# Optimization experiments

Measured on AMD Instinct MI355X. Metric: run time of the kernel, lower is better.

Reference implementation:

```python
import jax, jax.numpy as jnp
import numpy as np

NEG_SLOPE = 0.2  # PyG GATConv default negative_slope
EPS = 1e-16


def gat_conv(x, edge_index, W, att_src, att_dst, bias, heads, out_c, concat):
    """Faithful PyG GATConv forward (add_self_loops=True).
    x: [N, F_in], edge_index: [2, E] (row 0 = src, row 1 = dst),
    W: [heads*out_c, F_in], att_src/att_dst: [1, heads, out_c], bias: [out]
    """
    N = x.shape[0]
    loop = jnp.arange(N, dtype=edge_index.dtype)
    src = jnp.concatenate([edge_index[0], loop])
    dst = jnp.concatenate([edge_index[1], loop])

    h = (x @ W.T).reshape(N, heads, out_c)            # [N, H, C]
    a_src = jnp.sum(h * att_src, axis=-1)             # [N, H]
    a_dst = jnp.sum(h * att_dst, axis=-1)             # [N, H]

    e = jax.nn.leaky_relu(a_src[src] + a_dst[dst], NEG_SLOPE)   # [E+N, H]
    # numerically-stable segment softmax over incoming edges of dst
    m = jax.ops.segment_max(e, dst, num_segments=N)             # [N, H]
    p = jnp.exp(e - m[dst])
    denom = jax.ops.segment_sum(p, dst, num_segments=N)         # [N, H]
    alpha = p / (denom[dst] + EPS)                              # [E+N, H]

    out = jax.ops.segment_sum(h[src] * alpha[:, :, None], dst, num_segments=N)  # [N, H, C]
    out = out.reshape(N, heads * out_c) if concat else out.mean(axis=1)
    return out + bias


def setup_inputs() -> dict:
    key = jax.random.key(0)
    ks = jax.random.split(key, 11)
    N, E = 100_000, 1_600_000
    in_dim, hid, heads = 128, 64, 2
    s = 0.1
    x = jax.random.normal(ks[0], (N, in_dim), jnp.float32)
    edge_index_l2 = jax.random.randint(ks[1], (2, E), 0, N, dtype=jnp.int32)
    edge_index_l1 = jax.random.randint(ks[2], (2, E), 0, N, dtype=jnp.int32)
    # layer gat_l2: in_dim -> hid per head, heads=2, concat=True
    W2 = jax.random.normal(ks[3], (heads * hid, in_dim), jnp.float32) * s
    att_src2 = jax.random.normal(ks[4], (1, heads, hid), jnp.float32) * s
    att_dst2 = jax.random.normal(ks[5], (1, heads, hid), jnp.float32) * s
    b2 = jnp.zeros((heads * hid,), jnp.float32)
    # layer gat_l1: hid*heads -> hid, 1 head, concat=False
    W1 = jax.random.normal(ks[6], (hid, heads * hid), jnp.float32) * s
    att_src1 = jax.random.normal(ks[7], (1, 1, hid), jnp.float32) * s
    att_dst1 = jax.random.normal(ks[8], (1, 1, hid), jnp.float32) * s
    b1 = jnp.zeros((hid,), jnp.float32)
    return {
        "x": x,
        "edge_index_l1": edge_index_l1,
        "edge_index_l2": edge_index_l2,
        "W2": W2, "att_src2": att_src2, "att_dst2": att_dst2, "b2": b2,
        "W1": W1, "att_src1": att_src1, "att_dst1": att_dst1, "b1": b1,
    }


def reference(x, edge_index_l1, edge_index_l2, W2, att_src2, att_dst2, b2,
              W1, att_src1, att_dst1, b1):
    h = jax.nn.elu(gat_conv(x, edge_index_l2, W2, att_src2, att_dst2, b2,
                            heads=2, out_c=64, concat=True))    # [N, 128]
    h = jax.nn.elu(gat_conv(h, edge_index_l1, W1, att_src1, att_dst1, b1,
                            heads=1, out_c=64, concat=False))   # [N, 64]
    return h
```

## Files before the change

kernel.cpp:

```cpp
#include <hip/hip_runtime.h>
#include <hip/hip_bf16.h>
#include <math.h>

#define LRELU_SLOPE 0.2f
#define EPS 1e-16f
#define BUCK_SHIFT 8
#define BUCK_NODES 256
#define MAXBUCK 512

typedef __hip_bfloat16 bf16;
typedef __attribute__((ext_vector_type(8))) short bf16x8;
typedef __attribute__((ext_vector_type(4))) float f32x4;

__device__ inline float lrelu(float v) { return v > 0.f ? v : LRELU_SLOPE * v; }
__device__ inline float bflo(unsigned u) { return __uint_as_float(u << 16); }
__device__ inline float bfhi(unsigned u) { return __uint_as_float(u & 0xffff0000u); }
__device__ inline short f2bf(float f) {
  bf16 t = __float2bfloat16(f);
  return *reinterpret_cast<short*>(&t);
}

__global__ void convert_w(const float* __restrict__ W2, unsigned short* __restrict__ Wb2,
                          const float* __restrict__ W1, unsigned short* __restrict__ Wb1) {
  int idx = blockIdx.x * blockDim.x + threadIdx.x;
  if (idx < 16384) {
    Wb2[idx] = (unsigned short)f2bf(W2[idx]);
  } else {
    int i = idx - 16384;
    if (i < 8192) Wb1[i] = (unsigned short)f2bf(W1[i]);
  }
}

template <int EPB>
__global__ __launch_bounds__(256) void partition_kernel(const int* __restrict__ ei, int E,
                                                        int* __restrict__ gcur,
                                                        int2* __restrict__ part, int cap,
                                                        int nbuck) {
  __shared__ int cnt[MAXBUCK];
  __shared__ int sbase[MAXBUCK];
  const int tid = threadIdx.x;
  for (int t = tid; t < nbuck; t += 256) cnt[t] = 0;
  __syncthreads();
  const int e0 = blockIdx.x * EPB;
  constexpr int KPT = EPB / 256;
  int sv[KPT], dv[KPT];
#pragma unroll
  for (int k = 0; k < KPT; k++) {
    int e = e0 + tid + k * 256;
    if (e < E) {
      sv[k] = ei[e];
      dv[k] = ei[E + e];
      atomicAdd(&cnt[dv[k] >> BUCK_SHIFT], 1);
    } else {
      dv[k] = -1;
    }
  }
  __syncthreads();
  for (int t = tid; t < nbuck; t += 256) {
    int c = cnt[t];
    if (c) sbase[t] = atomicAdd(&gcur[t], c);
    cnt[t] = 0;
  }
  __syncthreads();
#pragma unroll
  for (int k = 0; k < KPT; k++) {
    if (dv[k] >= 0) {
      int b = dv[k] >> BUCK_SHIFT;
      int pos = sbase[b] + atomicAdd(&cnt[b], 1);
      if (pos < cap) part[(size_t)b * cap + pos] = make_int2(sv[k], dv[k]);
    }
  }
}

template <int H>
__global__ __launch_bounds__(256) void csr_build_kernel(
    const int2* __restrict__ part, const int* __restrict__ gcur, int cap,
    const float* __restrict__ asrc, const float* __restrict__ adst, int* __restrict__ eidx,
    float* __restrict__ pcsr, int* __restrict__ rowbeg, int* __restrict__ rowend, int N) {
  extern __shared__ char smem[];
  int* s_s = (int*)smem;
  unsigned short* s_d8 = (unsigned short*)(s_s + cap);
  int* hist = (int*)(s_d8 + cap);
  int* escan = hist + 256;
  int* cur = escan + 256;
  float* s_ad = (float*)(cur + 256);

  const int b = blockIdx.x;
  const int tid = threadIdx.x;
  const int nb0 = b << BUCK_SHIFT;
  const int nn = min(BUCK_NODES, N - nb0);
  const int cnt = min(gcur[b], cap);
  const int B = b * cap;

  hist[tid] = 0;
  cur[tid] = 0;
  for (int t = tid; t < nn * H; t += 256) s_ad[t] = adst[(size_t)nb0 * H + t];
  __syncthreads();
  for (int i = tid; i < cnt; i += 256) {
    int2 pr = part[(size_t)B + i];
    s_s[i] = pr.x;
    int d8 = pr.y & (BUCK_NODES - 1);
    s_d8[i] = (unsigned short)d8;
    atomicAdd(&hist[d8], 1);
  }
  __syncthreads();
  escan[tid] = hist[tid];
  __syncthreads();
  for (int off = 1; off < 256; off <<= 1) {
    int t = (tid >= off) ? escan[tid - off] : 0;
    __syncthreads();
    escan[tid] += t;
    __syncthreads();
  }
  if (tid < nn) {
    rowbeg[nb0 + tid] = B + escan[tid] - hist[tid];
    rowend[nb0 + tid] = B + escan[tid];
  }
  __syncthreads();
  for (int i = tid; i < cnt; i += 256) {
    int d8 = s_d8[i];
    int slot = B + (escan[d8] - hist[d8]) + atomicAdd(&cur[d8], 1);
    int s = s_s[i];
    eidx[slot] = s;
    if constexpr (H == 2) {
      float2 a = *(const float2*)&asrc[2 * (size_t)s];
      float2 ad = *(const float2*)&s_ad[2 * d8];
      float2 pv;
      pv.x = __expf(lrelu(a.x + ad.x));
      pv.y = __expf(lrelu(a.y + ad.y));
      *(float2*)&pcsr[2 * (size_t)slot] = pv;
    } else {
      pcsr[slot] = __expf(lrelu(asrc[s] + s_ad[d8]));
    }
  }
}

template <int M, int H, bool SPLIT, typename Tin>
__global__ __launch_bounds__(256) void gemm_att_mfma(
    const Tin* __restrict__ x, const unsigned short* __restrict__ Wb,
    const float* __restrict__ atts, const float* __restrict__ attd, bf16* __restrict__ h,
    float* __restrict__ asrc, float* __restrict__ adst, int N) {
  constexpr int K = 128;
  constexpr int NF = M / 16;
  const int wid = threadIdx.x >> 6;
  const int lane = threadIdx.x & 63;
  const int r0 = blockIdx.x * 64 + wid * 16;
  if (r0 >= N) return;
  const int colb = lane & 15;
  const int kgrp = lane >> 4;
  const size_t arow = (size_t)min(r0 + colb, N - 1);

  f32x4 acc[NF];
#pragma unroll
  for (int f = 0; f < NF; f++) acc[f] = (f32x4){0.f, 0.f, 0.f, 0.f};

#pragma unroll
  for (int k0 = 0; k0 < K; k0 += 32) {
    const int kb = k0 + kgrp * 8;
    bf16x8 ahi, alo;
    if constexpr (SPLIT) {
      const float* xp = (const float*)x + arow * K + kb;
      float4 l0 = *(const float4*)xp;
      float4 l1 = *(const float4*)(xp + 4);
      float xv[8] = {l0.x, l0.y, l0.z, l0.w, l1.x, l1.y, l1.z, l1.w};
#pragma unroll
      for (int j = 0; j < 8; j++) {
        short hb = f2bf(xv[j]);
        ahi[j] = hb;
        float hf = __uint_as_float(((unsigned)(unsigned short)hb) << 16);
        alo[j] = f2bf(xv[j] - hf);
      }
    } else {
      ahi = *(const bf16x8*)((const unsigned short*)x + arow * K + kb);
    }
#pragma unroll
    for (int f = 0; f < NF; f++) {
      bf16x8 b = *(const bf16x8*)(Wb + (size_t)(f * 16 + colb) * K + kb);
      if constexpr (SPLIT)
        acc[f] = __builtin_amdgcn_mfma_f32_16x16x32_bf16(alo, b, acc[f], 0, 0, 0);
      acc[f] = __builtin_amdgcn_mfma_f32_16x16x32_bf16(ahi, b, acc[f], 0, 0, 0);
    }
  }

#pragma unroll
  for (int r = 0; r < 4; r++) {
    const int row = r0 + kgrp * 4 + r;
    const bool ok = row < N;
    float s0 = 0.f, d0 = 0.f, s1 = 0.f, d1 = 0.f;
#pragma unroll
    for (int f = 0; f < NF; f++) {
      float v = acc[f][r];
      int c = f * 16 + colb;
      if (ok) h[(size_t)row * M + c] = __float2bfloat16(v);
      float av = atts[c], dv = attd[c];
      if (H == 2 && f >= NF / 2) {
        s1 += v * av;
        d1 += v * dv;
      } else {
        s0 += v * av;
        d0 += v * dv;
      }
    }
#pragma unroll
    for (int off = 1; off < 16; off <<= 1) {
      s0 += __shfl_xor(s0, off);
      d0 += __shfl_xor(d0, off);
      if (H == 2) {
        s1 += __shfl_xor(s1, off);
        d1 += __shfl_xor(d1, off);
      }
    }
    if (ok && colb == 0) {
      if (H == 2) {
        asrc[2 * (size_t)row] = s0;
        asrc[2 * (size_t)row + 1] = s1;
        adst[2 * (size_t)row] = d0;
        adst[2 * (size_t)row + 1] = d1;
      } else {
        asrc[row] = s0;
        adst[row] = d0;
      }
    }
  }
}

__global__ void gather2_kernel(const bf16* __restrict__ h, const float* __restrict__ asrc,
                               const float* __restrict__ adst, const int* __restrict__ rowbeg,
                               const int* __restrict__ rowend, const int* __restrict__ eidx,
                               const float2* __restrict__ pcsr, const float* __restrict__ bias,
                               bf16* __restrict__ outp, int N) {
  long long gt = (long long)blockIdx.x * blockDim.x + threadIdx.x;
  int n = (int)(gt >> 6);
  int lane = threadIdx.x & 63;
  if (n >= N) return;
  int start = rowbeg[n];
  int end = rowend[n];
  const float2 as = *(const float2*)&asrc[2 * (size_t)n];
  const float2 ad = *(const float2*)&adst[2 * (size_t)n];
  float p0 = __expf(lrelu(as.x + ad.x));
  float p1 = __expf(lrelu(as.y + ad.y));
  float den0 = p0, den1 = p1;
  const bool h0 = lane < 32;
  float p = h0 ? p0 : p1;
  unsigned hv = *(const unsigned*)&h[(size_t)n * 128 + 2 * lane];
  float acc0 = p * bflo(hv), acc1 = p * bfhi(hv);
  int j = start;
  for (; j + 3 < end; j += 4) {
    int sA = eidx[j], sB = eidx[j + 1], sC = eidx[j + 2], sD = eidx[j + 3];
    float2 pA = pcsr[j], pB = pcsr[j + 1], pC = pcsr[j + 2], pD = pcsr[j + 3];
    unsigned hA = *(const unsigned*)&h[(size_t)sA * 128 + 2 * lane];
    unsigned hB = *(const unsigned*)&h[(size_t)sB * 128 + 2 * lane];
    unsigned hC = *(const unsigned*)&h[(size_t)sC * 128 + 2 * lane];
    unsigned hD = *(const unsigned*)&h[(size_t)sD * 128 + 2 * lane];
    den0 += (pA.x + pB.x) + (pC.x + pD.x);
    den1 += (pA.y + pB.y) + (pC.y + pD.y);
    float pa = h0 ? pA.x : pA.y;
    float pb = h0 ? pB.x : pB.y;
    float pc = h0 ? pC.x : pC.y;
    float pd = h0 ? pD.x : pD.y;
    acc0 += (pa * bflo(hA) + pb * bflo(hB)) + (pc * bflo(hC) + pd * bflo(hD));
    acc1 += (pa * bfhi(hA) + pb * bfhi(hB)) + (pc * bfhi(hC) + pd * bfhi(hD));
  }
  for (; j < end; j++) {
    int sA = eidx[j];
    float2 pA = pcsr[j];
    unsigned hA = *(const unsigned*)&h[(size_t)sA * 128 + 2 * lane];
    den0 += pA.x;
    den1 += pA.y;
    float pa = h0 ? pA.x : pA.y;
    acc0 += pa * bflo(hA);
    acc1 += pa * bfhi(hA);
  }
  float den = (h0 ? den0 : den1) + EPS;
  int c = 2 * lane;
  float v0 = acc0 / den + bias[c];
  float v1 = acc1 / den + bias[c + 1];
  v0 = v0 > 0.f ? v0 : expm1f(v0);
  v1 = v1 > 0.f ? v1 : expm1f(v1);
  __hip_bfloat162 o;
  o.x = __float2bfloat16(v0);
  o.y = __float2bfloat16(v1);
  *(__hip_bfloat162*)&outp[(size_t)n * 128 + c] = o;
}

__global__ void gather1_kernel(const bf16* __restrict__ h, const float* __restrict__ asrc,
                               const float* __restrict__ adst, const int* __restrict__ rowbeg,
                               const int* __restrict__ rowend, const int* __restrict__ eidx,
                               const float* __restrict__ pcsr, const float* __restrict__ bias,
                               float* __restrict__ outp, int N) {
  long long gt = (long long)blockIdx.x * blockDim.x + threadIdx.x;
  int n = (int)(gt >> 6);
  int lane = threadIdx.x & 63;
  if (n >= N) return;
  int start = rowbeg[n];
  int end = rowend[n];
  float p = __expf(lrelu(asrc[n] + adst[n]));
  float den = p;
  float acc = p * __bfloat162float(h[(size_t)n * 64 + lane]);
  int j = start;
  for (; j + 3 < end; j += 4) {
    int sA = eidx[j], sB = eidx[j + 1], sC = eidx[j + 2], sD = eidx[j + 3];
    float pA = pcsr[j], pB = pcsr[j + 1], pC = pcsr[j + 2], pD = pcsr[j + 3];
    float hA = __bfloat162float(h[(size_t)sA * 64 + lane]);
    float hB = __bfloat162float(h[(size_t)sB * 64 + lane]);
    float hC = __bfloat162float(h[(size_t)sC * 64 + lane]);
    float hD = __bfloat162float(h[(size_t)sD * 64 + lane]);
    den += (pA + pB) + (pC + pD);
    acc += (pA * hA + pB * hB) + (pC * hC + pD * hD);
  }
  for (; j < end; j++) {
    int sA = eidx[j];
    float pA = pcsr[j];
    den += pA;
    acc += pA * __bfloat162float(h[(size_t)sA * 64 + lane]);
  }
  float v = acc / (den + EPS) + bias[lane];
  outp[(size_t)n * 64 + lane] = v > 0.f ? v : expm1f(v);
}

extern "C" void kernel_launch(void* const* d_in, const int* in_sizes, int n_in,
                              void* d_out, int out_size, void* d_ws, size_t ws_size,
                              hipStream_t stream) {
  const float* x = (const float*)d_in[0];
  const int* ei1 = (const int*)d_in[1];
  const int* ei2 = (const int*)d_in[2];
  const float* W2 = (const float*)d_in[3];
  const float* as2 = (const float*)d_in[4];
  const float* ad2 = (const float*)d_in[5];
  const float* b2 = (const float*)d_in[6];
  const float* W1 = (const float*)d_in[7];
  const float* as1 = (const float*)d_in[8];
  const float* ad1 = (const float*)d_in[9];
  const float* b1 = (const float*)d_in[10];
  float* out = (float*)d_out;

  const int N = in_sizes[0] / 128;
  const int E1 = in_sizes[1] / 2;
  const int E2 = in_sizes[2] / 2;
  const int Emax = E1 > E2 ? E1 : E2;
  const size_t Ns = (size_t)N;

  const int nbuck = (N + BUCK_NODES - 1) / BUCK_NODES;
  int lam = (Emax + nbuck - 1) / nbuck;
  int cap = lam + (lam >> 2) + 512;
  cap = (cap + 255) & ~(int)255;
  const size_t NC = (size_t)nbuck * cap;

  float* ws = (float*)d_ws;
  size_t o = 0;
  unsigned short* Wb2 = (unsigned short*)(ws + o); o += 8192;
  unsigned short* Wb1 = (unsigned short*)(ws + o); o += 4096;
  float* asrc2 = ws + o;  o += 2 * Ns;
  float* adst2 = ws + o;  o += 2 * Ns;
  float* asrc1 = ws + o;  o += Ns;
  float* adst1 = ws + o;  o += Ns;
  int* gcur2 = (int*)(ws + o);   o += (size_t)nbuck;
  int* gcur1 = (int*)(ws + o);   o += (size_t)nbuck;
  int* rowbeg2 = (int*)(ws + o); o += Ns;
  int* rowend2 = (int*)(ws + o); o += Ns;
  int* rowbeg1 = (int*)(ws + o); o += Ns;
  int* rowend1 = (int*)(ws + o); o += Ns;
  o = (o + 7) & ~(size_t)7;
  int2* part = (int2*)(ws + o);  o += 2 * NC;
  int* eidx = (int*)(ws + o);    o += NC;
  o = (o + 7) & ~(size_t)7;
  float* pcsr = ws + o;          o += 2 * NC;
  o = (o + 7) & ~(size_t)7;
  bf16* h2 = (bf16*)(ws + o);    o += 64 * Ns;
  bf16* h1 = h2;
  bf16* hin1 = (bf16*)(ws + o);  o += 64 * Ns;

  const size_t smem2 = (size_t)cap * 6 + 3 * 256 * 4 + 2 * 256 * 4 + 64;
  const size_t smem1 = (size_t)cap * 6 + 3 * 256 * 4 + 1 * 256 * 4 + 64;

  convert_w<<<(16384 + 8192 + 255) / 256, 256, 0, stream>>>(W2, Wb2, W1, Wb1);
  hipMemsetAsync(gcur2, 0, 2 * (size_t)nbuck * sizeof(int), stream);

  partition_kernel<4096><<<(E2 + 4095) / 4096, 256, 0, stream>>>(ei2, E2, gcur2, part, cap, nbuck);
  gemm_att_mfma<128, 2, true, float>
      <<<(N + 63) / 64, 256, 0, stream>>>(x, Wb2, as2, ad2, h2, asrc2, adst2, N);
  csr_build_kernel<2><<<nbuck, 256, smem2, stream>>>(part, gcur2, cap, asrc2, adst2, eidx, pcsr,
                                                     rowbeg2, rowend2, N);
  partition_kernel<4096><<<(E1 + 4095) / 4096, 256, 0, stream>>>(ei1, E1, gcur1, part, cap, nbuck);
  gather2_kernel<<<(N + 3) / 4, 256, 0, stream>>>(h2, asrc2, adst2, rowbeg2, rowend2, eidx,
                                                  (const float2*)pcsr, b2, hin1, N);

  gemm_att_mfma<64, 1, false, bf16>
      <<<(N + 63) / 64, 256, 0, stream>>>(hin1, Wb1, as1, ad1, h1, asrc1, adst1, N);
  csr_build_kernel<1><<<nbuck, 256, smem1, stream>>>(part, gcur1, cap, asrc1, adst1, eidx, pcsr,
                                                     rowbeg1, rowend1, N);
  gather1_kernel<<<(N + 3) / 4, 256, 0, stream>>>(h1, asrc1, adst1, rowbeg1, rowend1, eidx, pcsr,
                                                  b1, out, N);
}
```

Before: 343.1 us.

## Pack partition entries, pad CSR rows to eight, vectorize gathers

Partition entries are packed into a single int (src<<8 | local dst) instead of an int2, halving partition traffic and shared memory. CSR rows are padded to multiples of 8 with zero-weight dummy edges, so both gather kernels can use int4/float4 loads with no tail loop. The layer-1 gather now splits each wavefront into two halves over edges, with each lane handling two channels. Padding adds extra gather work and raises cap. Packing assumes source indices fit in 23 bits, and with cap reduced by 7*256 some edges may be dropped when a bucket overflows.

```diff
diff --git a/kernel.cpp b/kernel.cpp
--- a/kernel.cpp
+++ b/kernel.cpp
@@ -34,7 +34,7 @@
 template <int EPB>
 __global__ __launch_bounds__(256) void partition_kernel(const int* __restrict__ ei, int E,
                                                         int* __restrict__ gcur,
-                                                        int2* __restrict__ part, int cap,
+                                                        int* __restrict__ part, int cap,
                                                         int nbuck) {
   __shared__ int cnt[MAXBUCK];
   __shared__ int sbase[MAXBUCK];
@@ -67,29 +67,29 @@
     if (dv[k] >= 0) {
       int b = dv[k] >> BUCK_SHIFT;
       int pos = sbase[b] + atomicAdd(&cnt[b], 1);
-      if (pos < cap) part[(size_t)b * cap + pos] = make_int2(sv[k], dv[k]);
+      if (pos < cap) part[(size_t)b * cap + pos] = (sv[k] << 8) | (dv[k] & (BUCK_NODES - 1));
     }
   }
 }
 
 template <int H>
 __global__ __launch_bounds__(256) void csr_build_kernel(
-    const int2* __restrict__ part, const int* __restrict__ gcur, int cap,
+    const int* __restrict__ part, const int* __restrict__ gcur, int cap,
     const float* __restrict__ asrc, const float* __restrict__ adst, int* __restrict__ eidx,
     float* __restrict__ pcsr, int* __restrict__ rowbeg, int* __restrict__ rowend, int N) {
   extern __shared__ char smem[];
-  int* s_s = (int*)smem;
-  unsigned short* s_d8 = (unsigned short*)(s_s + cap);
-  int* hist = (int*)(s_d8 + cap);
-  int* escan = hist + 256;
-  int* cur = escan + 256;
+  int* s_sd = (int*)smem;
+  int* hist = (int*)(s_sd + cap);
+  int* histp = hist + 256;
+  int* escanp = histp + 256;
+  int* cur = escanp + 256;
   float* s_ad = (float*)(cur + 256);
 
   const int b = blockIdx.x;
   const int tid = threadIdx.x;
   const int nb0 = b << BUCK_SHIFT;
   const int nn = min(BUCK_NODES, N - nb0);
-  const int cnt = min(gcur[b], cap);
+  const int cnt = min(gcur[b], cap - 7 * BUCK_NODES);
   const int B = b * cap;
 
   hist[tid] = 0;
@@ -97,30 +97,31 @@
   for (int t = tid; t < nn * H; t += 256) s_ad[t] = adst[(size_t)nb0 * H + t];
   __syncthreads();
   for (int i = tid; i < cnt; i += 256) {
-    int2 pr = part[(size_t)B + i];
-    s_s[i] = pr.x;
-    int d8 = pr.y & (BUCK_NODES - 1);
-    s_d8[i] = (unsigned short)d8;
-    atomicAdd(&hist[d8], 1);
-  }
-  __syncthreads();
-  escan[tid] = hist[tid];
+    int pr = part[(size_t)B + i];
+    s_sd[i] = pr;
+    atomicAdd(&hist[pr & (BUCK_NODES - 1)], 1);
+  }
+  __syncthreads();
+  int hp = (hist[tid] + 7) & ~7;
+  histp[tid] = hp;
+  escanp[tid] = hp;
   __syncthreads();
   for (int off = 1; off < 256; off <<= 1) {
-    int t = (tid >= off) ? escan[tid - off] : 0;
+    int t = (tid >= off) ? escanp[tid - off] : 0;
     __syncthreads();
-    escan[tid] += t;
+    escanp[tid] += t;
     __syncthreads();
   }
   if (tid < nn) {
-    rowbeg[nb0 + tid] = B + escan[tid] - hist[tid];
-    rowend[nb0 + tid] = B + escan[tid];
+    rowbeg[nb0 + tid] = B + escanp[tid] - histp[tid];
+    rowend[nb0 + tid] = B + escanp[tid];
   }
   __syncthreads();
   for (int i = tid; i < cnt; i += 256) {
-    int d8 = s_d8[i];
-    int slot = B + (escan[d8] - hist[d8]) + atomicAdd(&cur[d8], 1);
-    int s = s_s[i];
+    int pr = s_sd[i];
+    int d8 = pr & (BUCK_NODES - 1);
+    int s = pr >> 8;
+    int slot = B + (escanp[d8] - histp[d8]) + atomicAdd(&cur[d8], 1);
     eidx[slot] = s;
     if constexpr (H == 2) {
       float2 a = *(const float2*)&asrc[2 * (size_t)s];
@@ -131,6 +132,17 @@
       *(float2*)&pcsr[2 * (size_t)slot] = pv;
     } else {
       pcsr[slot] = __expf(lrelu(asrc[s] + s_ad[d8]));
+    }
+  }
+  if (tid < nn) {
+    int base = B + escanp[tid] - histp[tid];
+    for (int k = hist[tid]; k < histp[tid]; k++) {
+      eidx[base + k] = nb0 + tid;
+      if constexpr (H == 2) {
+        *(float2*)&pcsr[2 * (size_t)(base + k)] = make_float2(0.f, 0.f);
+      } else {
+        pcsr[base + k] = 0.f;
+      }
     }
   }
 }
@@ -227,7 +239,7 @@
 __global__ void gather2_kernel(const bf16* __restrict__ h, const float* __restrict__ asrc,
                                const float* __restrict__ adst, const int* __restrict__ rowbeg,
                                const int* __restrict__ rowend, const int* __restrict__ eidx,
-                               const float2* __restrict__ pcsr, const float* __restrict__ bias,
+                               const float* __restrict__ pcsr, const float* __restrict__ bias,
                                bf16* __restrict__ outp, int N) {
   long long gt = (long long)blockIdx.x * blockDim.x + threadIdx.x;
   int n = (int)(gt >> 6);
@@ -244,32 +256,35 @@
   float p = h0 ? p0 : p1;
   unsigned hv = *(const unsigned*)&h[(size_t)n * 128 + 2 * lane];
   float acc0 = p * bflo(hv), acc1 = p * bfhi(hv);
-  int j = start;
-  for (; j + 3 < end; j += 4) {
-    int sA = eidx[j], sB = eidx[j + 1], sC = eidx[j + 2], sD = eidx[j + 3];
-    float2 pA = pcsr[j], pB = pcsr[j + 1], pC = pcsr[j + 2], pD = pcsr[j + 3];
-    unsigned hA = *(const unsigned*)&h[(size_t)sA * 128 + 2 * lane];
-    unsigned hB = *(const unsigned*)&h[(size_t)sB * 128 + 2 * lane];
-    unsigned hC = *(const unsigned*)&h[(size_t)sC * 128 + 2 * lane];
-    unsigned hD = *(const unsigned*)&h[(size_t)sD * 128 + 2 * lane];
-    den0 += (pA.x + pB.x) + (pC.x + pD.x);
-    den1 += (pA.y + pB.y) + (pC.y + pD.y);
-    float pa = h0 ? pA.x : pA.y;
-    float pb = h0 ? pB.x : pB.y;
-    float pc = h0 ? pC.x : pC.y;
-    float pd = h0 ? pD.x : pD.y;
-    acc0 += (pa * bflo(hA) + pb * bflo(hB)) + (pc * bflo(hC) + pd * bflo(hD));
-    acc1 += (pa * bfhi(hA) + pb * bfhi(hB)) + (pc * bfhi(hC) + pd * bfhi(hD));
-  }
-  for (; j < end; j++) {
-    int sA = eidx[j];
-    float2 pA = pcsr[j];
-    unsigned hA = *(const unsigned*)&h[(size_t)sA * 128 + 2 * lane];
-    den0 += pA.x;
-    den1 += pA.y;
-    float pa = h0 ? pA.x : pA.y;
-    acc0 += pa * bflo(hA);
-    acc1 += pa * bfhi(hA);
+  for (int j = start; j < end; j += 8) {
+    int4 ia = *(const int4*)&eidx[j];
+    int4 ib = *(const int4*)&eidx[j + 4];
+    float4 q0 = *(const float4*)&pcsr[2 * (size_t)j];
+    float4 q1 = *(const float4*)&pcsr[2 * (size_t)j + 4];
+    float4 q2 = *(const float4*)&pcsr[2 * (size_t)j + 8];
+    float4 q3 = *(const float4*)&pcsr[2 * (size_t)j + 12];
+    unsigned hA = *(const unsigned*)&h[(size_t)ia.x * 128 + 2 * lane];
+    unsigned hB = *(const unsigned*)&h[(size_t)ia.y * 128 + 2 * lane];
+    unsigned hC = *(const unsigned*)&h[(size_t)ia.z * 128 + 2 * lane];
+    unsigned hD = *(const unsigned*)&h[(size_t)ia.w * 128 + 2 * lane];
+    unsigned hE = *(const unsigned*)&h[(size_t)ib.x * 128 + 2 * lane];
+    unsigned hF = *(const unsigned*)&h[(size_t)ib.y * 128 + 2 * lane];
+    unsigned hG = *(const unsigned*)&h[(size_t)ib.z * 128 + 2 * lane];
+    unsigned hH = *(const unsigned*)&h[(size_t)ib.w * 128 + 2 * lane];
+    den0 += (q0.x + q0.z) + (q1.x + q1.z) + (q2.x + q2.z) + (q3.x + q3.z);
+    den1 += (q0.y + q0.w) + (q1.y + q1.w) + (q2.y + q2.w) + (q3.y + q3.w);
+    float pa = h0 ? q0.x : q0.y;
+    float pb = h0 ? q0.z : q0.w;
+    float pc = h0 ? q1.x : q1.y;
+    float pd = h0 ? q1.z : q1.w;
+    float pe = h0 ? q2.x : q2.y;
+    float pf = h0 ? q2.z : q2.w;
+    float pg = h0 ? q3.x : q3.y;
+    float ph = h0 ? q3.z : q3.w;
+    acc0 += (pa * bflo(hA) + pb * bflo(hB)) + (pc * bflo(hC) + pd * bflo(hD)) +
+            (pe * bflo(hE) + pf * bflo(hF)) + (pg * bflo(hG) + ph * bflo(hH));
+    acc1 += (pa * bfhi(hA) + pb * bfhi(hB)) + (pc * bfhi(hC) + pd * bfhi(hD)) +
+            (pe * bfhi(hE) + pf * bfhi(hF)) + (pg * bfhi(hG) + ph * bfhi(hH));
   }
   float den = (h0 ? den0 : den1) + EPS;
   int c = 2 * lane;
@@ -292,30 +307,36 @@
   int n = (int)(gt >> 6);
   int lane = threadIdx.x & 63;
   if (n >= N) return;
+  const int half = lane >> 5;
+  const int c = lane & 31;
   int start = rowbeg[n];
   int end = rowend[n];
-  float p = __expf(lrelu(asrc[n] + adst[n]));
-  float den = p;
-  float acc = p * __bfloat162float(h[(size_t)n * 64 + lane]);
-  int j = start;
-  for (; j + 3 < end; j += 4) {
-    int sA = eidx[j], sB = eidx[j + 1], sC = eidx[j + 2], sD = eidx[j + 3];
-    float pA = pcsr[j], pB = pcsr[j + 1], pC = pcsr[j + 2], pD = pcsr[j + 3];
-    float hA = __bfloat162float(h[(size_t)sA * 64 + lane]);
-    float hB = __bfloat162float(h[(size_t)sB * 64 + lane]);
-    float hC = __bfloat162float(h[(size_t)sC * 64 + lane]);
-    float hD = __bfloat162float(h[(size_t)sD * 64 + lane]);
-    den += (pA + pB) + (pC + pD);
-    acc += (pA * hA + pB * hB) + (pC * hC + pD * hD);
-  }
-  for (; j < end; j++) {
-    int sA = eidx[j];
-    float pA = pcsr[j];
-    den += pA;
-    acc += pA * __bfloat162float(h[(size_t)sA * 64 + lane]);
-  }
-  float v = acc / (den + EPS) + bias[lane];
-  outp[(size_t)n * 64 + lane] = v > 0.f ? v : expm1f(v);
+  float pself = __expf(lrelu(asrc[n] + adst[n]));
+  unsigned hv = *(const unsigned*)&h[(size_t)n * 64 + 2 * c];
+  float g = half ? 0.f : pself;
+  float den = g;
+  float acc0 = g * bflo(hv), acc1 = g * bfhi(hv);
+  for (int t = start + half * 4; t < end; t += 8) {
+    int4 ia = *(const int4*)&eidx[t];
+    float4 pa = *(const float4*)&pcsr[t];
+    unsigned hA = *(const unsigned*)&h[(size_t)ia.x * 64 + 2 * c];
+    unsigned hB = *(const unsigned*)&h[(size_t)ia.y * 64 + 2 * c];
+    unsigned hC = *(const unsigned*)&h[(size_t)ia.z * 64 + 2 * c];
+    unsigned hD = *(const unsigned*)&h[(size_t)ia.w * 64 + 2 * c];
+    den += (pa.x + pa.y) + (pa.z + pa.w);
+    acc0 += (pa.x * bflo(hA) + pa.y * bflo(hB)) + (pa.z * bflo(hC) + pa.w * bflo(hD));
+    acc1 += (pa.x * bfhi(hA) + pa.y * bfhi(hB)) + (pa.z * bfhi(hC) + pa.w * bfhi(hD));
+  }
+  den += __shfl_xor(den, 32);
+  acc0 += __shfl_xor(acc0, 32);
+  acc1 += __shfl_xor(acc1, 32);
+  float vden = den + EPS;
+  float2 bv = *(const float2*)&bias[2 * c];
+  float v0 = acc0 / vden + bv.x;
+  float v1 = acc1 / vden + bv.y;
+  v0 = v0 > 0.f ? v0 : expm1f(v0);
+  v1 = v1 > 0.f ? v1 : expm1f(v1);
+  if (!half) *(float2*)&outp[(size_t)n * 64 + 2 * c] = make_float2(v0, v1);
 }
 
 extern "C" void kernel_launch(void* const* d_in, const int* in_sizes, int n_in,
@@ -342,7 +363,7 @@
 
   const int nbuck = (N + BUCK_NODES - 1) / BUCK_NODES;
   int lam = (Emax + nbuck - 1) / nbuck;
-  int cap = lam + (lam >> 2) + 512;
+  int cap = lam + (lam >> 2) + 2048;
   cap = (cap + 255) & ~(int)255;
   const size_t NC = (size_t)nbuck * cap;
 
@@ -361,7 +382,7 @@
   int* rowbeg1 = (int*)(ws + o); o += Ns;
   int* rowend1 = (int*)(ws + o); o += Ns;
   o = (o + 7) & ~(size_t)7;
-  int2* part = (int2*)(ws + o);  o += 2 * NC;
+  int* part = (int*)(ws + o);    o += NC;
   int* eidx = (int*)(ws + o);    o += NC;
   o = (o + 7) & ~(size_t)7;
   float* pcsr = ws + o;          o += 2 * NC;
@@ -370,8 +391,8 @@
   bf16* h1 = h2;
   bf16* hin1 = (bf16*)(ws + o);  o += 64 * Ns;
 
-  const size_t smem2 = (size_t)cap * 6 + 3 * 256 * 4 + 2 * 256 * 4 + 64;
-  const size_t smem1 = (size_t)cap * 6 + 3 * 256 * 4 + 1 * 256 * 4 + 64;
+  const size_t smem2 = (size_t)cap * 4 + 4 * 256 * 4 + 2 * 256 * 4 + 64;
+  const size_t smem1 = (size_t)cap * 4 + 4 * 256 * 4 + 1 * 256 * 4 + 64;
 
   convert_w<<<(16384 + 8192 + 255) / 256, 256, 0, stream>>>(W2, Wb2, W1, Wb1);
   hipMemsetAsync(gcur2, 0, 2 * (size_t)nbuck * sizeof(int), stream);
@@ -382,8 +403,8 @@
   csr_build_kernel<2><<<nbuck, 256, smem2, stream>>>(part, gcur2, cap, asrc2, adst2, eidx, pcsr,
                                                      rowbeg2, rowend2, N);
   partition_kernel<4096><<<(E1 + 4095) / 4096, 256, 0, stream>>>(ei1, E1, gcur1, part, cap, nbuck);
-  gather2_kernel<<<(N + 3) / 4, 256, 0, stream>>>(h2, asrc2, adst2, rowbeg2, rowend2, eidx,
-                                                  (const float2*)pcsr, b2, hin1, N);
+  gather2_kernel<<<(N + 3) / 4, 256, 0, stream>>>(h2, asrc2, adst2, rowbeg2, rowend2, eidx, pcsr,
+                                                  b2, hin1, N);
 
   gemm_att_mfma<64, 1, false, bf16>
       <<<(N + 63) / 64, 256, 0, stream>>>(hin1, Wb1, as1, ad1, h1, asrc1, adst1, N);
```

Result: faster. 324.4 us (-5.5%).
